# Performance work log

Hardware: AMD Instinct MI355X
Metric: run time of the kernel (lower is better)

## Reference

```python
import jax, jax.numpy as jnp
import numpy as np

EMBED = 256
HEADS = 8
HEAD_DIM = EMBED // HEADS
K = 7          # kernel_size
DIL = 1        # dilation
PAD = DIL * (K - 1) // 2  # 3
B, H, W = 4, 56, 56


def setup_inputs() -> dict:
    key = jax.random.key(0)
    ks = jax.random.split(key, 9)
    d = {"x": jax.random.normal(ks[0], (B, H, W, EMBED), jnp.float32)}
    for i, name in enumerate(["wq", "wk", "wv", "wo"]):
        d[name] = jax.random.normal(ks[1 + i], (EMBED, EMBED), jnp.float32) * 0.02
    for i, name in enumerate(["bq", "bk", "bv", "bo"]):
        d[name] = jax.random.normal(ks[5 + i], (EMBED,), jnp.float32) * 0.02
    return d


def _unfold(t):
    # t: [N, d, H, W] -> [N, d, K*K, H, W]; zero padding (matches F.unfold),
    # so out-of-bounds neighbors contribute logit 0, NOT -inf (faithful to source).
    h, w = t.shape[2], t.shape[3]
    tp = jnp.pad(t, ((0, 0), (0, 0), (PAD, PAD), (PAD, PAD)))
    patches = [tp[:, :, i * DIL:i * DIL + h, j * DIL:j * DIL + w]
               for i in range(K) for j in range(K)]  # fixed K*K=49 offsets
    return jnp.stack(patches, axis=2)


def reference(x, wq, bq, wk, bk, wv, bv, wo, bo):
    b, h, w, c = x.shape
    scale = HEAD_DIM ** -0.5
    q = x @ wq.T + bq
    k = x @ wk.T + bk
    v = x @ wv.T + bv

    def to_nh(t):  # [B,H,W,C] -> [B*heads, head_dim, H, W]
        return t.reshape(b, h, w, HEADS, HEAD_DIM).transpose(0, 3, 4, 1, 2).reshape(b * HEADS, HEAD_DIM, h, w)

    q, k, v = to_nh(q), to_nh(k), to_nh(v)
    k_unf = _unfold(k)  # [N, d, K2, H, W]
    v_unf = _unfold(v)
    logits = jnp.einsum('ndhw,ndkhw->nkhw', q, k_unf) * scale  # [N, K2, H, W]
    attn = jax.nn.softmax(logits, axis=1)
    out = jnp.einsum('nkhw,ndkhw->ndhw', attn, v_unf)  # [N, d, H, W]
    out = out.reshape(b, HEADS, HEAD_DIM, h, w).transpose(0, 3, 4, 1, 2).reshape(b, h, w, c)
    return out @ wo.T + bo
```

## Files before the change

kernel.cpp:

```cpp
#include <hip/hip_runtime.h>

typedef unsigned int u32;
typedef unsigned short u16;
typedef __attribute__((ext_vector_type(8))) short bf16x8;
typedef __attribute__((ext_vector_type(4))) float f32x4;

#define T_TOK 12544
#define EMB   256
#define IMG   56
#define SCALE 0.17677669529663689f
#define HALO  196
#define KSTR  40
#define VTSTR 224
#define PSTR  232

__device__ __forceinline__ u32 bf16_rtne(float f) {
    u32 u = __builtin_bit_cast(u32, f);
    return (u + 0x7fffu + ((u >> 16) & 1u)) >> 16;
}
__device__ __forceinline__ float bf16_to_f(u32 h) { return __builtin_bit_cast(float, h << 16); }
__device__ __forceinline__ u32 pk2(float a, float b) {
    return bf16_rtne(a) | (bf16_rtne(b) << 16);
}

#define GLD16(g, l) __builtin_amdgcn_global_load_lds( \
    (const __attribute__((address_space(1))) u32*)(g), \
    (__attribute__((address_space(3))) u32*)(l), 16, 0, 0)

__global__ __launch_bounds__(256) void weight_convert(
    const float* __restrict__ wq, const float* __restrict__ wk,
    const float* __restrict__ wv, const float* __restrict__ wo,
    u16* __restrict__ bsh, u16* __restrict__ boh, u16* __restrict__ bol) {
    const int i = blockIdx.x * 256 + threadIdx.x;
    const int w = i >> 14, widx = i & 16383;
    const float* src = (w == 0) ? wq : (w == 1) ? wk : (w == 2) ? wv : wo;
    const float4 f = ((const float4*)src)[widx];
    const float vf[4] = {f.x, f.y, f.z, f.w};
    if (w < 3) {
        ushort4 hv;
        u16* hp = (u16*)&hv;
        #pragma unroll
        for (int c = 0; c < 4; ++c) hp[c] = (u16)bf16_rtne(vf[c]);
        ((ushort4*)bsh)[(w << 14) + widx] = hv;
    } else {
        ushort4 hv, lv;
        u16* hp = (u16*)&hv; u16* lp = (u16*)&lv;
        #pragma unroll
        for (int c = 0; c < 4; ++c) {
            const u32 h = bf16_rtne(vf[c]);
            hp[c] = (u16)h;
            lp[c] = (u16)bf16_rtne(vf[c] - bf16_to_f(h));
        }
        ((ushort4*)boh)[widx] = hv;
        ((ushort4*)bol)[widx] = lv;
    }
}

__global__ __launch_bounds__(256) void qkv_mfma(
    const float* __restrict__ x, const u16* __restrict__ bsh,
    const float* __restrict__ bq, const float* __restrict__ bk, const float* __restrict__ bv,
    u16* __restrict__ qb, u16* __restrict__ kb, u16* __restrict__ vb) {
    __shared__ __attribute__((aligned(16))) u16 sA[128 * 32];
    __shared__ __attribute__((aligned(16))) u16 sB[128 * 32];
    const int nBase = blockIdx.x * 128;
    const int mBase = blockIdx.y * 128;
    const int tid = threadIdx.x, wv = tid >> 6, ln = tid & 63;
    const int lrow = ln & 15, lqd = ln >> 4;
    const int wm = (wv & 1) * 64, wn = (wv >> 1) * 64;
    const int c0 = wv * 128 + ln, r0 = c0 >> 2, kc0 = c0 & 3;
    const int c1 = c0 + 64,       r1 = c1 >> 2, kc1 = c1 & 3;
    const size_t gA0 = (size_t)(mBase + r0) * EMB + kc0 * 8;
    const size_t gA1 = (size_t)(mBase + r1) * EMB + kc1 * 8;
    const size_t gB0 = (size_t)(nBase + r0) * EMB + kc0 * 8;
    const size_t gB1 = (size_t)(nBase + r1) * EMB + kc1 * 8;
    const int l0 = (wv * 128) * 8, l1 = (wv * 128 + 64) * 8;

    f32x4 acc[4][4];
    #pragma unroll
    for (int mi = 0; mi < 4; ++mi)
        #pragma unroll
        for (int ni = 0; ni < 4; ++ni)
            acc[mi][ni] = (f32x4){0.f, 0.f, 0.f, 0.f};

    for (int kt = 0; kt < 8; ++kt) {
        const int k0 = kt * 32;
        GLD16(bsh + gB0 + k0, sB + l0);
        GLD16(bsh + gB1 + k0, sB + l1);
        {
            const float4 f0 = *(const float4*)&x[gA0 + k0];
            const float4 f1 = *(const float4*)&x[gA0 + k0 + 4];
            const uint4 p = {pk2(f0.x, f0.y), pk2(f0.z, f0.w),
                             pk2(f1.x, f1.y), pk2(f1.z, f1.w)};
            *(uint4*)&sA[c0 * 8] = p;
        }
        {
            const float4 f0 = *(const float4*)&x[gA1 + k0];
            const float4 f1 = *(const float4*)&x[gA1 + k0 + 4];
            const uint4 p = {pk2(f0.x, f0.y), pk2(f0.z, f0.w),
                             pk2(f1.x, f1.y), pk2(f1.z, f1.w)};
            *(uint4*)&sA[c1 * 8] = p;
        }
        __syncthreads();
        bf16x8 af[4], bf[4];
        #pragma unroll
        for (int mi = 0; mi < 4; ++mi)
            af[mi] = *(const bf16x8*)&sA[(wm + mi * 16 + lrow) * 32 + lqd * 8];
        #pragma unroll
        for (int ni = 0; ni < 4; ++ni)
            bf[ni] = *(const bf16x8*)&sB[(wn + ni * 16 + lrow) * 32 + lqd * 8];
        #pragma unroll
        for (int mi = 0; mi < 4; ++mi)
            #pragma unroll
            for (int ni = 0; ni < 4; ++ni)
                acc[mi][ni] = __builtin_amdgcn_mfma_f32_16x16x32_bf16(af[mi], bf[ni], acc[mi][ni], 0, 0, 0);
        __syncthreads();
    }

    const int which = nBase >> 8;
    const float* bias = (which == 0) ? bq : (which == 1) ? bk : bv;
    u16* dst = (which == 0) ? qb : (which == 1) ? kb : vb;
    #pragma unroll
    for (int ni = 0; ni < 4; ++ni) {
        const int ncol = nBase + wn + ni * 16 + lrow;
        const int c = ncol & 255;
        const float bz = bias[c];
        #pragma unroll
        for (int mi = 0; mi < 4; ++mi) {
            #pragma unroll
            for (int r = 0; r < 4; ++r) {
                const int row = mBase + wm + mi * 16 + lqd * 4 + r;
                dst[(size_t)row * EMB + c] = (u16)bf16_rtne(acc[mi][ni][r] + bz);
            }
        }
    }
}

__global__ __launch_bounds__(256) void out_mfma(
    const u16* __restrict__ aoh, const u16* __restrict__ aol,
    const u16* __restrict__ boh, const u16* __restrict__ bol,
    const float* __restrict__ bo, float* __restrict__ out) {
    __shared__ __attribute__((aligned(16))) u16 sAh[64 * 32];
    __shared__ __attribute__((aligned(16))) u16 sAl[64 * 32];
    __shared__ __attribute__((aligned(16))) u16 sBh[64 * 32];
    __shared__ __attribute__((aligned(16))) u16 sBl[64 * 32];
    const int nBase = blockIdx.x * 64;
    const int mBase = blockIdx.y * 64;
    const int tid = threadIdx.x, wv = tid >> 6, ln = tid & 63;
    const int lrow = ln & 15, lqd = ln >> 4;
    const int rA = tid >> 2, kcA = tid & 3;
    const size_t gA = (size_t)(mBase + rA) * EMB + kcA * 8;
    const size_t gB = (size_t)(nBase + rA) * EMB + kcA * 8;
    const int lA = wv * 64 * 8;

    f32x4 acc[4];
    #pragma unroll
    for (int mi = 0; mi < 4; ++mi) acc[mi] = (f32x4){0.f, 0.f, 0.f, 0.f};

    for (int kt = 0; kt < 8; ++kt) {
        const int k0 = kt * 32;
        GLD16(aoh + gA + k0, sAh + lA);
        GLD16(aol + gA + k0, sAl + lA);
        GLD16(boh + gB + k0, sBh + lA);
        GLD16(bol + gB + k0, sBl + lA);
        __syncthreads();
        bf16x8 ah[4], al[4];
        #pragma unroll
        for (int mi = 0; mi < 4; ++mi) {
            ah[mi] = *(const bf16x8*)&sAh[(mi * 16 + lrow) * 32 + lqd * 8];
            al[mi] = *(const bf16x8*)&sAl[(mi * 16 + lrow) * 32 + lqd * 8];
        }
        const bf16x8 bh = *(const bf16x8*)&sBh[(wv * 16 + lrow) * 32 + lqd * 8];
        const bf16x8 bl = *(const bf16x8*)&sBl[(wv * 16 + lrow) * 32 + lqd * 8];
        #pragma unroll
        for (int mi = 0; mi < 4; ++mi) {
            acc[mi] = __builtin_amdgcn_mfma_f32_16x16x32_bf16(ah[mi], bh, acc[mi], 0, 0, 0);
            acc[mi] = __builtin_amdgcn_mfma_f32_16x16x32_bf16(al[mi], bh, acc[mi], 0, 0, 0);
            acc[mi] = __builtin_amdgcn_mfma_f32_16x16x32_bf16(ah[mi], bl, acc[mi], 0, 0, 0);
        }
        __syncthreads();
    }

    const int ncol = nBase + wv * 16 + lrow;
    const float bz = bo[ncol];
    #pragma unroll
    for (int mi = 0; mi < 4; ++mi) {
        #pragma unroll
        for (int r = 0; r < 4; ++r) {
            const int row = mBase + mi * 16 + lqd * 4 + r;
            out[(size_t)row * EMB + ncol] = acc[mi][r] + bz;
        }
    }
}

__global__ __launch_bounds__(256, 3) void attn_kernel(
    const u16* __restrict__ qb, const u16* __restrict__ kb, const u16* __restrict__ vb,
    u16* __restrict__ aoh, u16* __restrict__ aol) {
    __shared__ __attribute__((aligned(16))) u16 smem[25088];
    u16* sK  = smem;
    u16* sV1 = smem + 8960;
    u16* sVT = smem + 17920;
    u16* sP  = smem;

    const int tid = threadIdx.x;
    const int w = tid >> 6, ln = tid & 63;
    const int lrow = ln & 15, lqd = ln >> 4;
    const int img = blockIdx.z >> 3, head = blockIdx.z & 7;
    const int ty0 = blockIdx.y * 8, tx0 = blockIdx.x * 8;

    for (int i = tid; i < 1792; i += 256) {
        const int mv = (i >= 896) ? 1 : 0;
        const int ii = i - 896 * mv;
        const int p = ii >> 2, c = ii & 3;
        const int pyh = p / 14, pxh = p - pyh * 14;
        const int gy = ty0 - 3 + pyh, gx = tx0 - 3 + pxh;
        u16* dst = (mv ? sV1 : sK) + p * KSTR + c * 8;
        if (p < HALO && (unsigned)gy < 56u && (unsigned)gx < 56u) {
            const size_t tt = ((size_t)img * IMG + gy) * IMG + gx;
            *(uint4*)dst = *(const uint4*)((mv ? vb : kb) + tt * EMB + head * 32 + c * 8);
        } else {
            *(uint4*)dst = (uint4){0u, 0u, 0u, 0u};
        }
    }
    __syncthreads();

    for (int i = tid; i < 896; i += 256) {
        const int d = i & 31, ho = i >> 5;
        u32 pk[4];
        #pragma unroll
        for (int j = 0; j < 4; ++j) {
            const u32 a = sV1[(ho * 8 + 2 * j)     * KSTR + d];
            const u32 b = sV1[(ho * 8 + 2 * j + 1) * KSTR + d];
            pk[j] = a | (b << 16);
        }
        *(uint4*)&sVT[d * VTSTR + ho * 8] = *(uint4*)pk;
    }

    const int mpix = w * 16 + lrow;
    const int qpy = mpix >> 3, qpx = mpix & 7;
    const size_t qtok = ((size_t)img * IMG + ty0 + qpy) * IMG + tx0 + qpx;
    const bf16x8 aq = *(const bf16x8*)&qb[qtok * EMB + head * 32 + lqd * 8];

    f32x4 ct[13];
    #pragma unroll
    for (int t = 0; t < 13; ++t) ct[t] = (f32x4){0.f, 0.f, 0.f, 0.f};
    #pragma unroll
    for (int t = 0; t < 13; ++t) {
        const bf16x8 bk = *(const bf16x8*)&sK[(t * 16 + lrow) * KSTR + lqd * 8];
        ct[t] = __builtin_amdgcn_mfma_f32_16x16x32_bf16(aq, bk, ct[t], 0, 0, 0);
    }

    int pys[4], pxs[4];
    #pragma unroll
    for (int r = 0; r < 4; ++r) {
        const int row = lqd * 4 + r;
        pys[r] = 2 * w + (row >> 3);
        pxs[r] = row & 7;
    }
    float mr4[4] = {-1e30f, -1e30f, -1e30f, -1e30f};
    #pragma unroll
    for (int t = 0; t < 13; ++t) {
        const int col = t * 16 + lrow;
        const int hy = col / 14, hx = col - 14 * hy;
        const bool okc = (col < HALO);
        #pragma unroll
        for (int r = 0; r < 4; ++r) {
            const bool ok = ((unsigned)(hy - pys[r]) < 7u) &
                            ((unsigned)(hx - pxs[r]) < 7u) & okc;
            const float lv = ok ? ct[t][r] * SCALE : -1e30f;
            ct[t][r] = lv;
            mr4[r] = fmaxf(mr4[r], lv);
        }
    }
    #pragma unroll
    for (int r = 0; r < 4; ++r) {
        float m = mr4[r];
        m = fmaxf(m, __shfl_xor(m, 1));
        m = fmaxf(m, __shfl_xor(m, 2));
        m = fmaxf(m, __shfl_xor(m, 4));
        m = fmaxf(m, __shfl_xor(m, 8));
        mr4[r] = m;
    }
    float sr4[4] = {0.f, 0.f, 0.f, 0.f};
    #pragma unroll
    for (int t = 0; t < 13; ++t)
        #pragma unroll
        for (int r = 0; r < 4; ++r) {
            const float e = __expf(ct[t][r] - mr4[r]);
            ct[t][r] = e;
            sr4[r] += e;
        }
    #pragma unroll
    for (int r = 0; r < 4; ++r) {
        float s = sr4[r];
        s += __shfl_xor(s, 1);
        s += __shfl_xor(s, 2);
        s += __shfl_xor(s, 4);
        s += __shfl_xor(s, 8);
        sr4[r] = 1.0f / s;
    }

    __syncthreads();

    u16* sPw = sP + w * 16 * PSTR;
    #pragma unroll
    for (int t = 0; t < 13; ++t)
        #pragma unroll
        for (int r = 0; r < 4; ++r)
            sPw[(lqd * 4 + r) * PSTR + t * 16 + lrow] = (u16)bf16_rtne(ct[t][r]);
    #pragma unroll
    for (int z = 0; z < 4; ++z) {
        const int idx = z * 64 + ln;
        sPw[(idx >> 4) * PSTR + 208 + (idx & 15)] = 0;
    }

    f32x4 o0 = (f32x4){0.f, 0.f, 0.f, 0.f};
    f32x4 o1 = (f32x4){0.f, 0.f, 0.f, 0.f};
    #pragma unroll
    for (int ks = 0; ks < 7; ++ks) {
        const bf16x8 ap  = *(const bf16x8*)&sPw[lrow * PSTR + ks * 32 + lqd * 8];
        const bf16x8 bv0 = *(const bf16x8*)&sVT[lrow * VTSTR + ks * 32 + lqd * 8];
        const bf16x8 bv1 = *(const bf16x8*)&sVT[(16 + lrow) * VTSTR + ks * 32 + lqd * 8];
        o0 = __builtin_amdgcn_mfma_f32_16x16x32_bf16(ap, bv0, o0, 0, 0, 0);
        o1 = __builtin_amdgcn_mfma_f32_16x16x32_bf16(ap, bv1, o1, 0, 0, 0);
    }

    #pragma unroll
    for (int r = 0; r < 4; ++r) {
        const int row = lqd * 4 + r;
        const int opy = 2 * w + (row >> 3), opx = row & 7;
        const size_t ot = ((size_t)img * IMG + ty0 + opy) * IMG + tx0 + opx;
        const float inv = sr4[r];
        const float v0 = o0[r] * inv;
        const float v1 = o1[r] * inv;
        const size_t base = ot * EMB + head * 32;
        const u32 h0 = bf16_rtne(v0);
        aoh[base + lrow] = (u16)h0;
        aol[base + lrow] = (u16)bf16_rtne(v0 - bf16_to_f(h0));
        const u32 h1 = bf16_rtne(v1);
        aoh[base + 16 + lrow] = (u16)h1;
        aol[base + 16 + lrow] = (u16)bf16_rtne(v1 - bf16_to_f(h1));
    }
}

extern "C" void kernel_launch(void* const* d_in, const int* in_sizes, int n_in,
                              void* d_out, int out_size, void* d_ws, size_t ws_size,
                              hipStream_t stream) {
    const float* x  = (const float*)d_in[0];
    const float* wq = (const float*)d_in[1];
    const float* wk = (const float*)d_in[2];
    const float* wv = (const float*)d_in[3];
    const float* wo = (const float*)d_in[4];
    const float* bq = (const float*)d_in[5];
    const float* bk = (const float*)d_in[6];
    const float* bv = (const float*)d_in[7];
    const float* bo = (const float*)d_in[8];
    float* out = (float*)d_out;

    char* ws = (char*)d_ws;
    u16* qb  = (u16*)(ws);
    u16* kb  = (u16*)(ws +  6422528);
    u16* vb  = (u16*)(ws + 12845056);
    u16* aoh = (u16*)(ws + 19267584);
    u16* aol = (u16*)(ws + 25690112);
    u16* bsh = (u16*)(ws + 32112640);
    u16* boh = (u16*)(ws + 32505856);
    u16* bol = (u16*)(ws + 32636928);

    weight_convert<<<256, 256, 0, stream>>>(wq, wk, wv, wo, bsh, boh, bol);
    qkv_mfma<<<dim3(6, 98), 256, 0, stream>>>(x, bsh, bq, bk, bv, qb, kb, vb);
    attn_kernel<<<dim3(7, 7, 32), 256, 0, stream>>>(qb, kb, vb, aoh, aol);
    out_mfma<<<dim3(4, 196), 256, 0, stream>>>(aoh, aol, boh, bol, bo, out);
}
```

Before: 133.8 us.

## Fuse weight conversion into GEMMs, double K-step qkv, transpose V during load

Removes the separate weight_convert kernel: qkv_mfma and out_mfma now read fp32 weights directly and convert them to bf16 (hi/lo split for wo) in registers using the hardware bf16 pack intrinsic. The qkv loop processes two 32-wide K slices per barrier pair, halving syncs, and the attention kernel scatters V transposed straight into LDS, dropping the staging buffer and one barrier while shrinking shared memory. This saves a kernel launch and workspace traffic, but every GEMM block redoes the weight conversion and the transposed V stores are scalar 16-bit LDS writes with possible bank conflicts.

```diff
diff --git a/kernel.cpp b/kernel.cpp
--- a/kernel.cpp
+++ b/kernel.cpp
@@ -1,4 +1,5 @@
 #include <hip/hip_runtime.h>
+#include <hip/hip_bf16.h>
 
 typedef unsigned int u32;
 typedef unsigned short u16;
@@ -19,61 +20,39 @@
     return (u + 0x7fffu + ((u >> 16) & 1u)) >> 16;
 }
 __device__ __forceinline__ float bf16_to_f(u32 h) { return __builtin_bit_cast(float, h << 16); }
-__device__ __forceinline__ u32 pk2(float a, float b) {
-    return bf16_rtne(a) | (bf16_rtne(b) << 16);
+__device__ __forceinline__ u32 pk2hw(float a, float b) {
+    __hip_bfloat162 h = __float22bfloat162_rn(make_float2(a, b));
+    u32 r; __builtin_memcpy(&r, &h, 4); return r;
 }
 
 #define GLD16(g, l) __builtin_amdgcn_global_load_lds( \
     (const __attribute__((address_space(1))) u32*)(g), \
     (__attribute__((address_space(3))) u32*)(l), 16, 0, 0)
 
-__global__ __launch_bounds__(256) void weight_convert(
-    const float* __restrict__ wq, const float* __restrict__ wk,
-    const float* __restrict__ wv, const float* __restrict__ wo,
-    u16* __restrict__ bsh, u16* __restrict__ boh, u16* __restrict__ bol) {
-    const int i = blockIdx.x * 256 + threadIdx.x;
-    const int w = i >> 14, widx = i & 16383;
-    const float* src = (w == 0) ? wq : (w == 1) ? wk : (w == 2) ? wv : wo;
-    const float4 f = ((const float4*)src)[widx];
-    const float vf[4] = {f.x, f.y, f.z, f.w};
-    if (w < 3) {
-        ushort4 hv;
-        u16* hp = (u16*)&hv;
-        #pragma unroll
-        for (int c = 0; c < 4; ++c) hp[c] = (u16)bf16_rtne(vf[c]);
-        ((ushort4*)bsh)[(w << 14) + widx] = hv;
-    } else {
-        ushort4 hv, lv;
-        u16* hp = (u16*)&hv; u16* lp = (u16*)&lv;
-        #pragma unroll
-        for (int c = 0; c < 4; ++c) {
-            const u32 h = bf16_rtne(vf[c]);
-            hp[c] = (u16)h;
-            lp[c] = (u16)bf16_rtne(vf[c] - bf16_to_f(h));
-        }
-        ((ushort4*)boh)[widx] = hv;
-        ((ushort4*)bol)[widx] = lv;
-    }
-}
-
 __global__ __launch_bounds__(256) void qkv_mfma(
-    const float* __restrict__ x, const u16* __restrict__ bsh,
+    const float* __restrict__ x,
+    const float* __restrict__ wq, const float* __restrict__ wk, const float* __restrict__ wv,
     const float* __restrict__ bq, const float* __restrict__ bk, const float* __restrict__ bv,
     u16* __restrict__ qb, u16* __restrict__ kb, u16* __restrict__ vb) {
-    __shared__ __attribute__((aligned(16))) u16 sA[128 * 32];
-    __shared__ __attribute__((aligned(16))) u16 sB[128 * 32];
+    __shared__ __attribute__((aligned(16))) u16 sA[2 * 128 * 32];
+    __shared__ __attribute__((aligned(16))) u16 sB[2 * 128 * 32];
     const int nBase = blockIdx.x * 128;
     const int mBase = blockIdx.y * 128;
-    const int tid = threadIdx.x, wv = tid >> 6, ln = tid & 63;
+    const int which = nBase >> 8;
+    const int colBase = nBase & 255;
+    const float* w    = (which == 0) ? wq : (which == 1) ? wk : wv;
+    const float* bias = (which == 0) ? bq : (which == 1) ? bk : bv;
+    u16* dst          = (which == 0) ? qb : (which == 1) ? kb : vb;
+
+    const int tid = threadIdx.x, wv2 = tid >> 6, ln = tid & 63;
     const int lrow = ln & 15, lqd = ln >> 4;
-    const int wm = (wv & 1) * 64, wn = (wv >> 1) * 64;
-    const int c0 = wv * 128 + ln, r0 = c0 >> 2, kc0 = c0 & 3;
-    const int c1 = c0 + 64,       r1 = c1 >> 2, kc1 = c1 & 3;
+    const int wm = (wv2 & 1) * 64, wn = (wv2 >> 1) * 64;
+    const int c0 = wv2 * 128 + ln, r0 = c0 >> 2, kc0 = c0 & 3;
+    const int c1 = c0 + 64,        r1 = c1 >> 2, kc1 = c1 & 3;
     const size_t gA0 = (size_t)(mBase + r0) * EMB + kc0 * 8;
     const size_t gA1 = (size_t)(mBase + r1) * EMB + kc1 * 8;
-    const size_t gB0 = (size_t)(nBase + r0) * EMB + kc0 * 8;
-    const size_t gB1 = (size_t)(nBase + r1) * EMB + kc1 * 8;
-    const int l0 = (wv * 128) * 8, l1 = (wv * 128 + 64) * 8;
+    const size_t gB0 = (size_t)(colBase + r0) * EMB + kc0 * 8;
+    const size_t gB1 = (size_t)(colBase + r1) * EMB + kc1 * 8;
 
     f32x4 acc[4][4];
     #pragma unroll
@@ -82,47 +61,63 @@
         for (int ni = 0; ni < 4; ++ni)
             acc[mi][ni] = (f32x4){0.f, 0.f, 0.f, 0.f};
 
-    for (int kt = 0; kt < 8; ++kt) {
-        const int k0 = kt * 32;
-        GLD16(bsh + gB0 + k0, sB + l0);
-        GLD16(bsh + gB1 + k0, sB + l1);
-        {
-            const float4 f0 = *(const float4*)&x[gA0 + k0];
-            const float4 f1 = *(const float4*)&x[gA0 + k0 + 4];
-            const uint4 p = {pk2(f0.x, f0.y), pk2(f0.z, f0.w),
-                             pk2(f1.x, f1.y), pk2(f1.z, f1.w)};
-            *(uint4*)&sA[c0 * 8] = p;
-        }
-        {
-            const float4 f0 = *(const float4*)&x[gA1 + k0];
-            const float4 f1 = *(const float4*)&x[gA1 + k0 + 4];
-            const uint4 p = {pk2(f0.x, f0.y), pk2(f0.z, f0.w),
-                             pk2(f1.x, f1.y), pk2(f1.z, f1.w)};
-            *(uint4*)&sA[c1 * 8] = p;
+    for (int kt2 = 0; kt2 < 4; ++kt2) {
+        #pragma unroll
+        for (int t = 0; t < 2; ++t) {
+            const int k0 = kt2 * 64 + t * 32;
+            const int lb = t * 4096;
+            {
+                const float4 f0 = *(const float4*)&x[gA0 + k0];
+                const float4 f1 = *(const float4*)&x[gA0 + k0 + 4];
+                const uint4 p = {pk2hw(f0.x, f0.y), pk2hw(f0.z, f0.w),
+                                 pk2hw(f1.x, f1.y), pk2hw(f1.z, f1.w)};
+                *(uint4*)&sA[lb + c0 * 8] = p;
+            }
+            {
+                const float4 f0 = *(const float4*)&x[gA1 + k0];
+                const float4 f1 = *(const float4*)&x[gA1 + k0 + 4];
+                const uint4 p = {pk2hw(f0.x, f0.y), pk2hw(f0.z, f0.w),
+                                 pk2hw(f1.x, f1.y), pk2hw(f1.z, f1.w)};
+                *(uint4*)&sA[lb + c1 * 8] = p;
+            }
+            {
+                const float4 f0 = *(const float4*)&w[gB0 + k0];
+                const float4 f1 = *(const float4*)&w[gB0 + k0 + 4];
+                const uint4 p = {pk2hw(f0.x, f0.y), pk2hw(f0.z, f0.w),
+                                 pk2hw(f1.x, f1.y), pk2hw(f1.z, f1.w)};
+                *(uint4*)&sB[lb + c0 * 8] = p;
+            }
+            {
+                const float4 f0 = *(const float4*)&w[gB1 + k0];
+                const float4 f1 = *(const float4*)&w[gB1 + k0 + 4];
+                const uint4 p = {pk2hw(f0.x, f0.y), pk2hw(f0.z, f0.w),
+                                 pk2hw(f1.x, f1.y), pk2hw(f1.z, f1.w)};
+                *(uint4*)&sB[lb + c1 * 8] = p;
+            }
         }
         __syncthreads();
-        bf16x8 af[4], bf[4];
-        #pragma unroll
-        for (int mi = 0; mi < 4; ++mi)
-            af[mi] = *(const bf16x8*)&sA[(wm + mi * 16 + lrow) * 32 + lqd * 8];
-        #pragma unroll
-        for (int ni = 0; ni < 4; ++ni)
-            bf[ni] = *(const bf16x8*)&sB[(wn + ni * 16 + lrow) * 32 + lqd * 8];
-        #pragma unroll
-        for (int mi = 0; mi < 4; ++mi)
+        #pragma unroll
+        for (int t = 0; t < 2; ++t) {
+            const int lb = t * 4096;
+            bf16x8 af[4], bf[4];
+            #pragma unroll
+            for (int mi = 0; mi < 4; ++mi)
+                af[mi] = *(const bf16x8*)&sA[lb + (wm + mi * 16 + lrow) * 32 + lqd * 8];
             #pragma unroll
             for (int ni = 0; ni < 4; ++ni)
-                acc[mi][ni] = __builtin_amdgcn_mfma_f32_16x16x32_bf16(af[mi], bf[ni], acc[mi][ni], 0, 0, 0);
+                bf[ni] = *(const bf16x8*)&sB[lb + (wn + ni * 16 + lrow) * 32 + lqd * 8];
+            #pragma unroll
+            for (int mi = 0; mi < 4; ++mi)
+                #pragma unroll
+                for (int ni = 0; ni < 4; ++ni)
+                    acc[mi][ni] = __builtin_amdgcn_mfma_f32_16x16x32_bf16(af[mi], bf[ni], acc[mi][ni], 0, 0, 0);
+        }
         __syncthreads();
     }
 
-    const int which = nBase >> 8;
-    const float* bias = (which == 0) ? bq : (which == 1) ? bk : bv;
-    u16* dst = (which == 0) ? qb : (which == 1) ? kb : vb;
     #pragma unroll
     for (int ni = 0; ni < 4; ++ni) {
-        const int ncol = nBase + wn + ni * 16 + lrow;
-        const int c = ncol & 255;
+        const int c = colBase + wn + ni * 16 + lrow;
         const float bz = bias[c];
         #pragma unroll
         for (int mi = 0; mi < 4; ++mi) {
@@ -137,8 +132,8 @@
 
 __global__ __launch_bounds__(256) void out_mfma(
     const u16* __restrict__ aoh, const u16* __restrict__ aol,
-    const u16* __restrict__ boh, const u16* __restrict__ bol,
-    const float* __restrict__ bo, float* __restrict__ out) {
+    const float* __restrict__ wo, const float* __restrict__ bo,
+    float* __restrict__ out) {
     __shared__ __attribute__((aligned(16))) u16 sAh[64 * 32];
     __shared__ __attribute__((aligned(16))) u16 sAl[64 * 32];
     __shared__ __attribute__((aligned(16))) u16 sBh[64 * 32];
@@ -160,8 +155,19 @@
         const int k0 = kt * 32;
         GLD16(aoh + gA + k0, sAh + lA);
         GLD16(aol + gA + k0, sAl + lA);
-        GLD16(boh + gB + k0, sBh + lA);
-        GLD16(bol + gB + k0, sBl + lA);
+        {
+            const float4 f0 = *(const float4*)&wo[gB + k0];
+            const float4 f1 = *(const float4*)&wo[gB + k0 + 4];
+            const uint4 ph = {pk2hw(f0.x, f0.y), pk2hw(f0.z, f0.w),
+                              pk2hw(f1.x, f1.y), pk2hw(f1.z, f1.w)};
+            const uint4 pl = {
+                pk2hw(f0.x - bf16_to_f(ph.x & 0xffffu), f0.y - bf16_to_f(ph.x >> 16)),
+                pk2hw(f0.z - bf16_to_f(ph.y & 0xffffu), f0.w - bf16_to_f(ph.y >> 16)),
+                pk2hw(f1.x - bf16_to_f(ph.z & 0xffffu), f1.y - bf16_to_f(ph.z >> 16)),
+                pk2hw(f1.z - bf16_to_f(ph.w & 0xffffu), f1.w - bf16_to_f(ph.w >> 16))};
+            *(uint4*)&sBh[tid * 8] = ph;
+            *(uint4*)&sBl[tid * 8] = pl;
+        }
         __syncthreads();
         bf16x8 ah[4], al[4];
         #pragma unroll
@@ -195,11 +201,10 @@
 __global__ __launch_bounds__(256, 3) void attn_kernel(
     const u16* __restrict__ qb, const u16* __restrict__ kb, const u16* __restrict__ vb,
     u16* __restrict__ aoh, u16* __restrict__ aol) {
-    __shared__ __attribute__((aligned(16))) u16 smem[25088];
-    u16* sK  = smem;
-    u16* sV1 = smem + 8960;
-    u16* sVT = smem + 17920;
-    u16* sP  = smem;
+    __shared__ __attribute__((aligned(16))) u16 smem[22016];
+    u16* sVT = smem;
+    u16* sK  = smem + 7168;
+    u16* sP  = smem + 7168;
 
     const int tid = threadIdx.x;
     const int w = tid >> 6, ln = tid & 63;
@@ -213,32 +218,40 @@
         const int p = ii >> 2, c = ii & 3;
         const int pyh = p / 14, pxh = p - pyh * 14;
         const int gy = ty0 - 3 + pyh, gx = tx0 - 3 + pxh;
-        u16* dst = (mv ? sV1 : sK) + p * KSTR + c * 8;
-        if (p < HALO && (unsigned)gy < 56u && (unsigned)gx < 56u) {
-            const size_t tt = ((size_t)img * IMG + gy) * IMG + gx;
-            *(uint4*)dst = *(const uint4*)((mv ? vb : kb) + tt * EMB + head * 32 + c * 8);
+        const bool ok = (p < HALO) & ((unsigned)gy < 56u) & ((unsigned)gx < 56u);
+        if (!mv) {
+            u16* dstk = sK + p * KSTR + c * 8;
+            if (ok) {
+                const size_t tt = ((size_t)img * IMG + gy) * IMG + gx;
+                *(uint4*)dstk = *(const uint4*)(kb + tt * EMB + head * 32 + c * 8);
+            } else {
+                *(uint4*)dstk = (uint4){0u, 0u, 0u, 0u};
+            }
         } else {
-            *(uint4*)dst = (uint4){0u, 0u, 0u, 0u};
-        }
-    }
-    __syncthreads();
-
-    for (int i = tid; i < 896; i += 256) {
-        const int d = i & 31, ho = i >> 5;
-        u32 pk[4];
-        #pragma unroll
-        for (int j = 0; j < 4; ++j) {
-            const u32 a = sV1[(ho * 8 + 2 * j)     * KSTR + d];
-            const u32 b = sV1[(ho * 8 + 2 * j + 1) * KSTR + d];
-            pk[j] = a | (b << 16);
-        }
-        *(uint4*)&sVT[d * VTSTR + ho * 8] = *(uint4*)pk;
+            u16* dv = sVT + (c * 8) * VTSTR + p;
+            if (ok) {
+                const size_t tt = ((size_t)img * IMG + gy) * IMG + gx;
+                const uint4 u = *(const uint4*)(vb + tt * EMB + head * 32 + c * 8);
+                dv[0 * VTSTR] = (u16)(u.x & 0xffffu);
+                dv[1 * VTSTR] = (u16)(u.x >> 16);
+                dv[2 * VTSTR] = (u16)(u.y & 0xffffu);
+                dv[3 * VTSTR] = (u16)(u.y >> 16);
+                dv[4 * VTSTR] = (u16)(u.z & 0xffffu);
+                dv[5 * VTSTR] = (u16)(u.z >> 16);
+                dv[6 * VTSTR] = (u16)(u.w & 0xffffu);
+                dv[7 * VTSTR] = (u16)(u.w >> 16);
+            } else {
+                #pragma unroll
+                for (int j = 0; j < 8; ++j) dv[j * VTSTR] = 0;
+            }
+        }
     }
 
     const int mpix = w * 16 + lrow;
     const int qpy = mpix >> 3, qpx = mpix & 7;
     const size_t qtok = ((size_t)img * IMG + ty0 + qpy) * IMG + tx0 + qpx;
     const bf16x8 aq = *(const bf16x8*)&qb[qtok * EMB + head * 32 + lqd * 8];
+    __syncthreads();
 
     f32x4 ct[13];
     #pragma unroll
@@ -362,12 +375,8 @@
     u16* vb  = (u16*)(ws + 12845056);
     u16* aoh = (u16*)(ws + 19267584);
     u16* aol = (u16*)(ws + 25690112);
-    u16* bsh = (u16*)(ws + 32112640);
-    u16* boh = (u16*)(ws + 32505856);
-    u16* bol = (u16*)(ws + 32636928);
-
-    weight_convert<<<256, 256, 0, stream>>>(wq, wk, wv, wo, bsh, boh, bol);
-    qkv_mfma<<<dim3(6, 98), 256, 0, stream>>>(x, bsh, bq, bk, bv, qb, kb, vb);
+
+    qkv_mfma<<<dim3(6, 98), 256, 0, stream>>>(x, wq, wk, wv, bq, bk, bv, qb, kb, vb);
     attn_kernel<<<dim3(7, 7, 32), 256, 0, stream>>>(qb, kb, vb, aoh, aol);
-    out_mfma<<<dim3(4, 196), 256, 0, stream>>>(aoh, aol, boh, bol, bo, out);
-}
+    out_mfma<<<dim3(4, 196), 256, 0, stream>>>(aoh, aol, wo, bo, out);
+}
```

New measurement: 137.1 us. 1.02x slower.
